# Kernel optimization log

Measured on AMD Instinct MI355X. Metric: run time of the kernel, lower is better.

## Reference

```python
import jax, jax.numpy as jnp
import numpy as np
import math

D_MODEL = 1024
NUM_HEADS = 16
D_K = D_MODEL // NUM_HEADS
NUM_BUCKETS = 32
MAX_DISTANCE = 512  # PositionalEncoding max_len


def _relative_position_bucket(relative_position):
    # Faithful to the torch code: both signs add num_buckets//2 (==16), rp==0 adds 0.
    half = NUM_BUCKETS // 2            # 16
    max_exact = NUM_BUCKETS // 4       # 8
    base = (relative_position > 0).astype(jnp.int32) * half \
         + (relative_position < 0).astype(jnp.int32) * half
    arp = jnp.abs(relative_position)
    is_small = arp < max_exact
    safe = jnp.maximum(arp, 1).astype(jnp.float32)  # avoid log(0); masked by is_small anyway
    large = max_exact + (jnp.log(safe / max_exact)
                         / math.log(MAX_DISTANCE / max_exact)
                         * (half - max_exact)).astype(jnp.int32)  # trunc == torch .long()
    large = jnp.minimum(large, half - 1)
    return base + jnp.where(is_small, arp, large)


def compute_bias(rel_bias_table, seq_length):
    ctx = jnp.arange(seq_length, dtype=jnp.int32)[:, None]
    mem = jnp.arange(seq_length, dtype=jnp.int32)[None, :]
    buckets = _relative_position_bucket(mem - ctx)        # [S, S]
    values = rel_bias_table[buckets]                       # [S, S, H]
    return jnp.transpose(values, (2, 0, 1))[None]          # [1, H, S, S]


def setup_inputs() -> dict:
    key = jax.random.key(0)
    ks = jax.random.split(key, 12)
    B, S, D = 2, 2048, D_MODEL
    scale = 1.0 / math.sqrt(D)
    inp = {
        "query": jax.random.normal(ks[0], (B, S, D), jnp.float32),
        "key": jax.random.normal(ks[1], (B, S, D), jnp.float32),
        "value": jax.random.normal(ks[2], (B, S, D), jnp.float32),
        "Wq": jax.random.normal(ks[3], (D, D), jnp.float32) * scale,
        "bq": jnp.zeros((D,), jnp.float32),
        "Wk": jax.random.normal(ks[4], (D, D), jnp.float32) * scale,
        "bk": jnp.zeros((D,), jnp.float32),
        "Wv": jax.random.normal(ks[5], (D, D), jnp.float32) * scale,
        "bv": jnp.zeros((D,), jnp.float32),
        "Wo": jax.random.normal(ks[6], (D, D), jnp.float32) * scale,
        "bo": jnp.zeros((D,), jnp.float32),
        "rel_bias_table": jax.random.normal(ks[7], (NUM_BUCKETS, NUM_HEADS), jnp.float32) * 0.1,
    }
    return inp


def reference(query, key, value, Wq, bq, Wk, bk, Wv, bv, Wo, bo, rel_bias_table):
    B, Sq, D = query.shape
    Sk = key.shape[1]
    H, dk = NUM_HEADS, D_K
    q = (query @ Wq + bq).reshape(B, Sq, H, dk)
    k = (key @ Wk + bk).reshape(B, Sk, H, dk)
    v = (value @ Wv + bv).reshape(B, Sk, H, dk)
    scores = jnp.einsum('bqhd,bkhd->bhqk', q, k) / math.sqrt(dk)  # [B,H,Sq,Sk]
    position_bias = compute_bias(rel_bias_table, max(Sq, Sk))[:, :, :Sq, :Sk]
    scores = scores + position_bias  # broadcast over batch (torch expand)
    attn_weights = jax.nn.softmax(scores, axis=-1)
    # dropout is identity in eval / p=0
    context = jnp.einsum('bhqk,bkhd->bqhd', attn_weights, v).reshape(B, Sq, D)
    output = context @ Wo + bo
    pb = jnp.broadcast_to(position_bias, (B, H, Sq, Sk))
    return output, attn_weights, pb
```

## Files before the change

### kernel.cpp

```cpp
#include <hip/hip_runtime.h>
#include <hip/hip_bf16.h>

#define BN 2
#define SEQ 2048
#define DM 1024
#define NH 16
#define DK 64

using f32x4  = __attribute__((ext_vector_type(4))) float;
using bf16x8 = __attribute__((ext_vector_type(8))) __bf16;
using short8 = __attribute__((ext_vector_type(8))) short;

static_assert(sizeof(bf16x8) == 16, "bf16x8 must be 16B");

#define MFMA16(a, b, c) __builtin_amdgcn_mfma_f32_16x16x32_bf16(a, b, c, 0, 0, 0)

__device__ __forceinline__ unsigned short f2b(float f) {
    __hip_bfloat16 h = __float2bfloat16(f);
    return __builtin_bit_cast(unsigned short, h);
}

__device__ __forceinline__ bf16x8 load_bf8(const unsigned short* p) {
    short8 s = *reinterpret_cast<const short8*>(p);
    return __builtin_bit_cast(bf16x8, s);
}

__global__ void bias_table_kernel(const float* __restrict__ rel,
                                  float* __restrict__ bias_val) {
    int idx = blockIdx.x * 256 + threadIdx.x;
    if (idx >= NH * 4095) return;
    int h = idx / 4095;
    int dd = idx - h * 4095;
    int d = dd - 2047;
    int a = d < 0 ? -d : d;
    int bucket;
    if (a == 0) bucket = 0;
    else if (a < 8) bucket = 16 + a;
    else {
        int k = (a >= 14) + (a >= 23) + (a >= 39) + (a >= 64) +
                (a >= 108) + (a >= 182) + (a >= 305);
        bucket = 24 + k;
    }
    bias_val[h * 4095 + dd] = rel[bucket * NH + h];
}

__global__ __launch_bounds__(256) void wtrans_kernel(
        const float* __restrict__ W0, const float* __restrict__ W1,
        const float* __restrict__ W2, const float* __restrict__ W3,
        unsigned short* __restrict__ T0, unsigned short* __restrict__ T1,
        unsigned short* __restrict__ T2, unsigned short* __restrict__ T3) {
    constexpr int P = 68;
    __shared__ unsigned short lt[64 * P];
    const int mz = blockIdx.z;
    const float* W = mz == 0 ? W0 : mz == 1 ? W1 : mz == 2 ? W2 : W3;
    unsigned short* T = mz == 0 ? T0 : mz == 1 ? T1 : mz == 2 ? T2 : T3;
    const int k0 = blockIdx.x * 64, n0 = blockIdx.y * 64;
    const int tid = threadIdx.x;
#pragma unroll
    for (int p = 0; p < 4; ++p) {
        int r = p * 16 + (tid >> 4);
        int c = (tid & 15) * 4;
        float4 vv = *(const float4*)&W[(size_t)(k0 + r) * DM + n0 + c];
#pragma unroll
        for (int j = 0; j < 4; ++j) {
            int n = c + j;
            float x = j == 0 ? vv.x : j == 1 ? vv.y : j == 2 ? vv.z : vv.w;
            lt[n * P + (r ^ ((n & 7) << 3))] = f2b(x);
        }
    }
    __syncthreads();
#pragma unroll
    for (int p = 0; p < 2; ++p) {
        int rn = p * 32 + (tid >> 3);
        int ck = (tid & 7) * 8;
        int ckx = ck ^ ((rn & 7) << 3);
        ushort4 a0 = *(ushort4*)&lt[rn * P + ckx];
        ushort4 a1 = *(ushort4*)&lt[rn * P + ckx + 4];
        *(ushort4*)&T[(size_t)(n0 + rn) * DM + k0 + ck] = a0;
        *(ushort4*)&T[(size_t)(n0 + rn) * DM + k0 + ck + 4] = a1;
    }
}

__global__ __launch_bounds__(256) void qkv_gemm(
        const float* __restrict__ Aq, const float* __restrict__ Ak, const float* __restrict__ Av,
        const unsigned short* __restrict__ Wtq, const unsigned short* __restrict__ Wtk,
        const unsigned short* __restrict__ Wtv,
        const float* __restrict__ bq, const float* __restrict__ bk, const float* __restrict__ bv,
        unsigned short* __restrict__ Qp, unsigned short* __restrict__ Kh,
        unsigned short* __restrict__ Vt) {
    constexpr int KP = 40;
    __shared__ unsigned short la[128 * KP];
    __shared__ unsigned short lb[128 * KP];
    const int mat = blockIdx.z;
    const float* A = mat == 0 ? Aq : mat == 1 ? Ak : Av;
    const unsigned short* Wt = mat == 0 ? Wtq : mat == 1 ? Wtk : Wtv;
    const float* bias = mat == 0 ? bq : mat == 1 ? bk : bv;
    const float outscale = mat == 0 ? 0.125f : 1.0f;
    const int tid = threadIdx.x;
    const int m0 = blockIdx.y * 128, n0 = blockIdx.x * 128;
    const int lane = tid & 63, wid = tid >> 6;
    const int wm0 = (wid >> 1) * 64, wn0 = (wid & 1) * 64;
    const int l15 = lane & 15, l4 = lane >> 4;
    f32x4 acc[4][4] = {};

    for (int kt = 0; kt < 32; ++kt) {
        const int k0 = kt * 32;
#pragma unroll
        for (int i = 0; i < 4; ++i) {
            int idx = tid + i * 256;
            int row = idx >> 3, c4 = (idx & 7) * 4;
            float4 v = *(const float4*)(A + (size_t)(m0 + row) * DM + k0 + c4);
            ushort4 u; u.x = f2b(v.x); u.y = f2b(v.y); u.z = f2b(v.z); u.w = f2b(v.w);
            *(ushort4*)&la[row * KP + c4] = u;
        }
#pragma unroll
        for (int i = 0; i < 2; ++i) {
            int idx = tid + i * 256;
            int row = idx >> 2, c8 = (idx & 3) * 8;
            *(int4*)&lb[row * KP + c8] =
                *(const int4*)&Wt[(size_t)(n0 + row) * DM + k0 + c8];
        }
        __syncthreads();
        bf16x8 af[4], bfv[4];
#pragma unroll
        for (int m = 0; m < 4; ++m)
            af[m] = load_bf8(&la[(wm0 + m * 16 + l15) * KP + l4 * 8]);
#pragma unroll
        for (int n = 0; n < 4; ++n)
            bfv[n] = load_bf8(&lb[(wn0 + n * 16 + l15) * KP + l4 * 8]);
#pragma unroll
        for (int m = 0; m < 4; ++m)
#pragma unroll
            for (int n = 0; n < 4; ++n)
                acc[m][n] = MFMA16(af[m], bfv[n], acc[m][n]);
        __syncthreads();
    }

    float bv4[4];
#pragma unroll
    for (int n = 0; n < 4; ++n) bv4[n] = bias[n0 + wn0 + n * 16 + l15];
#pragma unroll
    for (int m = 0; m < 4; ++m) {
#pragma unroll
        for (int n = 0; n < 4; ++n) {
            int gcol = n0 + wn0 + n * 16 + l15;
#pragma unroll
            for (int r = 0; r < 4; ++r) {
                int grow = m0 + wm0 + m * 16 + l4 * 4 + r;
                float val = (acc[m][n][r] + bv4[n]) * outscale;
                unsigned short ob = f2b(val);
                int b = grow >> 11, s = grow & 2047;
                int hh = gcol >> 6, dl = gcol & 63;
                if (mat == 0) {
                    Qp[(size_t)grow * DM + gcol] = ob;
                } else if (mat == 1) {
                    Kh[(((size_t)(b * NH + hh) * SEQ + s) << 6) + dl] = ob;
                } else {
                    Vt[(((size_t)(b * NH + hh) * DK + dl) << 11) + s] = ob;
                }
            }
        }
    }
}

__global__ __launch_bounds__(256) void o_gemm(
        const unsigned short* __restrict__ Actx, const unsigned short* __restrict__ Wto,
        const float* __restrict__ bo, float* __restrict__ out) {
    constexpr int KP = 40;
    __shared__ unsigned short la[64 * KP];
    __shared__ unsigned short lb[128 * KP];
    const int tid = threadIdx.x;
    const int m0 = blockIdx.y * 64, n0 = blockIdx.x * 128;
    const int lane = tid & 63, wid = tid >> 6;
    const int wm0 = (wid >> 1) * 32, wn0 = (wid & 1) * 64;
    const int l15 = lane & 15, l4 = lane >> 4;
    f32x4 acc[2][4] = {};

    for (int kt = 0; kt < 32; ++kt) {
        const int k0 = kt * 32;
        {
            int row = tid >> 2, c8 = (tid & 3) * 8;
            *(int4*)&la[row * KP + c8] =
                *(const int4*)&Actx[(size_t)(m0 + row) * DM + k0 + c8];
        }
#pragma unroll
        for (int i = 0; i < 2; ++i) {
            int idx = tid + i * 256;
            int row = idx >> 2, c8 = (idx & 3) * 8;
            *(int4*)&lb[row * KP + c8] =
                *(const int4*)&Wto[(size_t)(n0 + row) * DM + k0 + c8];
        }
        __syncthreads();
        bf16x8 af[2], bfv[4];
#pragma unroll
        for (int m = 0; m < 2; ++m)
            af[m] = load_bf8(&la[(wm0 + m * 16 + l15) * KP + l4 * 8]);
#pragma unroll
        for (int n = 0; n < 4; ++n)
            bfv[n] = load_bf8(&lb[(wn0 + n * 16 + l15) * KP + l4 * 8]);
#pragma unroll
        for (int m = 0; m < 2; ++m)
#pragma unroll
            for (int n = 0; n < 4; ++n)
                acc[m][n] = MFMA16(af[m], bfv[n], acc[m][n]);
        __syncthreads();
    }

#pragma unroll
    for (int m = 0; m < 2; ++m)
#pragma unroll
        for (int n = 0; n < 4; ++n) {
            int gcol = n0 + wn0 + n * 16 + l15;
            float bb = bo[gcol];
#pragma unroll
            for (int r = 0; r < 4; ++r) {
                int grow = m0 + wm0 + m * 16 + l4 * 4 + r;
                out[(size_t)grow * DM + gcol] = acc[m][n][r] + bb;
            }
        }
}

__global__ __launch_bounds__(256) void attn3_kernel(
        const unsigned short* __restrict__ Qp, const unsigned short* __restrict__ Kh,
        const unsigned short* __restrict__ Vt, const float* __restrict__ bias_val,
        float* __restrict__ attn_out, float* __restrict__ pb_out,
        unsigned short* __restrict__ ctx) {
    __shared__ float bias_lds[2112];
    __shared__ float wtile[4][16 * 36];
    const int tid = threadIdx.x;
    const int lane = tid & 63, wid = tid >> 6;
    const int l15 = lane & 15, l4 = lane >> 4;
    const int bid = (blockIdx.x & 7) * 128 + (blockIdx.x >> 3);
    const int qb = bid & 31;
    const int h = (bid >> 5) & 15;
    const int b = bid >> 9;
    const int q0 = qb * 64;
    const int qw = q0 + wid * 16;

    {
        const float* bp = bias_val + h * 4095 + (2047 - (q0 + 63));
        for (int i = tid; i < 2111; i += 256) bias_lds[i] = bp[i];
    }
    __syncthreads();

    const unsigned short* qbase = Qp + (size_t)(b * SEQ + qw + l15) * DM + h * DK;
    bf16x8 qa0 = load_bf8(qbase + l4 * 8);
    bf16x8 qa1 = load_bf8(qbase + 32 + l4 * 8);

    const unsigned short* kbase = Kh + (((size_t)(b * NH + h) * SEQ) << 6);
    const int bbase = 63 - wid * 16 - l4 * 4;

    float m[4], l[4];
#pragma unroll
    for (int r = 0; r < 4; ++r) { m[r] = -3e38f; l[r] = 0.f; }

    for (int c0 = 0; c0 < SEQ; c0 += 32) {
        const unsigned short* kp = kbase + ((size_t)(c0 + l15) << 6);
        bf16x8 k00 = load_bf8(kp + l4 * 8);
        bf16x8 k01 = load_bf8(kp + 32 + l4 * 8);
        bf16x8 k10 = load_bf8(kp + (16 << 6) + l4 * 8);
        bf16x8 k11 = load_bf8(kp + (16 << 6) + 32 + l4 * 8);
        f32x4 a0 = {}, a1 = {};
        a0 = MFMA16(qa0, k00, a0); a0 = MFMA16(qa1, k01, a0);
        a1 = MFMA16(qa0, k10, a1); a1 = MFMA16(qa1, k11, a1);
#pragma unroll
        for (int r = 0; r < 4; ++r) {
            float s0 = a0[r] + bias_lds[c0 + l15 + bbase - r];
            float s1 = a1[r] + bias_lds[c0 + 16 + l15 + bbase - r];
            float cm = fmaxf(s0, s1);
            if (cm > m[r]) { l[r] *= __expf(m[r] - cm); m[r] = cm; }
            l[r] += __expf(s0 - m[r]) + __expf(s1 - m[r]);
        }
    }
#pragma unroll
    for (int off = 1; off < 16; off <<= 1) {
#pragma unroll
        for (int r = 0; r < 4; ++r) {
            float om = __shfl_xor(m[r], off);
            float ol = __shfl_xor(l[r], off);
            float M = fmaxf(m[r], om);
            l[r] = l[r] * __expf(m[r] - M) + ol * __expf(om - M);
            m[r] = M;
        }
    }
    float invl[4];
#pragma unroll
    for (int r = 0; r < 4; ++r) invl[r] = 1.0f / l[r];

    float* wt = wtile[wid];
    float* abase = attn_out + ((size_t)((b * NH + h) * SEQ + qw)) * SEQ;
    float* pbase = pb_out + ((size_t)((b * NH + h) * SEQ + qw)) * SEQ;
    const unsigned short* vbase = Vt + (((size_t)(b * NH + h) * DK) << 11);
    f32x4 cacc[4] = {};

    bf16x8 k00, k01, k10, k11;
    {
        const unsigned short* kp = kbase + ((size_t)l15 << 6);
        k00 = load_bf8(kp + l4 * 8);
        k01 = load_bf8(kp + 32 + l4 * 8);
        k10 = load_bf8(kp + (16 << 6) + l4 * 8);
        k11 = load_bf8(kp + (16 << 6) + 32 + l4 * 8);
    }
    const int srow = lane >> 2, scg = (lane & 3) * 8;
    for (int c0 = 0; c0 < SEQ; c0 += 32) {
        f32x4 a0 = {}, a1 = {};
        a0 = MFMA16(qa0, k00, a0); a0 = MFMA16(qa1, k01, a0);
        a1 = MFMA16(qa0, k10, a1); a1 = MFMA16(qa1, k11, a1);
        const int cn = (c0 + 32) & (SEQ - 1);
        const unsigned short* kp = kbase + ((size_t)(cn + l15) << 6);
        k00 = load_bf8(kp + l4 * 8);
        k01 = load_bf8(kp + 32 + l4 * 8);
        k10 = load_bf8(kp + (16 << 6) + l4 * 8);
        k11 = load_bf8(kp + (16 << 6) + 32 + l4 * 8);
        bf16x8 vv0 = load_bf8(vbase + ((size_t)(0 * 16 + l15) << 11) + c0 + l4 * 8);
        bf16x8 vv1 = load_bf8(vbase + ((size_t)(1 * 16 + l15) << 11) + c0 + l4 * 8);
        bf16x8 vv2 = load_bf8(vbase + ((size_t)(2 * 16 + l15) << 11) + c0 + l4 * 8);
        bf16x8 vv3 = load_bf8(vbase + ((size_t)(3 * 16 + l15) << 11) + c0 + l4 * 8);
#pragma unroll
        for (int r = 0; r < 4; ++r) {
            int row = l4 * 4 + r;
            float w0 = __expf(a0[r] + bias_lds[c0 + l15 + bbase - r] - m[r]) * invl[r];
            float w1 = __expf(a1[r] + bias_lds[c0 + 16 + l15 + bbase - r] - m[r]) * invl[r];
            wt[row * 36 + l15] = w0;
            wt[row * 36 + 16 + l15] = w1;
        }
        asm volatile("s_waitcnt lgkmcnt(0)" ::: "memory");
        __builtin_amdgcn_sched_barrier(0);
        {
            float4 v0 = *(const float4*)&wt[srow * 36 + scg];
            float4 v1 = *(const float4*)&wt[srow * 36 + scg + 4];
            float* gp = abase + (size_t)srow * SEQ + c0 + scg;
            *(float4*)gp = v0;
            *(float4*)(gp + 4) = v1;
        }
        {
            const int ib = c0 + scg + bbase + l4 * 4 - srow;
            float4 p0, p1;
            p0.x = bias_lds[ib + 0]; p0.y = bias_lds[ib + 1];
            p0.z = bias_lds[ib + 2]; p0.w = bias_lds[ib + 3];
            p1.x = bias_lds[ib + 4]; p1.y = bias_lds[ib + 5];
            p1.z = bias_lds[ib + 6]; p1.w = bias_lds[ib + 7];
            float* gp = pbase + (size_t)srow * SEQ + c0 + scg;
            *(float4*)gp = p0;
            *(float4*)(gp + 4) = p1;
        }
        float4 pA = *(const float4*)&wt[l15 * 36 + l4 * 8];
        float4 pB = *(const float4*)&wt[l15 * 36 + l4 * 8 + 4];
        short8 ps;
        ps[0] = (short)f2b(pA.x); ps[1] = (short)f2b(pA.y);
        ps[2] = (short)f2b(pA.z); ps[3] = (short)f2b(pA.w);
        ps[4] = (short)f2b(pB.x); ps[5] = (short)f2b(pB.y);
        ps[6] = (short)f2b(pB.z); ps[7] = (short)f2b(pB.w);
        bf16x8 pf = __builtin_bit_cast(bf16x8, ps);
        cacc[0] = MFMA16(pf, vv0, cacc[0]);
        cacc[1] = MFMA16(pf, vv1, cacc[1]);
        cacc[2] = MFMA16(pf, vv2, cacc[2]);
        cacc[3] = MFMA16(pf, vv3, cacc[3]);
        asm volatile("s_waitcnt lgkmcnt(0)" ::: "memory");
        __builtin_amdgcn_sched_barrier(0);
    }
#pragma unroll
    for (int d0 = 0; d0 < 4; ++d0)
#pragma unroll
        for (int r = 0; r < 4; ++r)
            ctx[(size_t)(b * SEQ + qw + l4 * 4 + r) * DM + h * DK + d0 * 16 + l15] =
                f2b(cacc[d0][r]);
}

extern "C" void kernel_launch(void* const* d_in, const int* in_sizes, int n_in,
                              void* d_out, int out_size, void* d_ws, size_t ws_size,
                              hipStream_t stream) {
    const float* query = (const float*)d_in[0];
    const float* key   = (const float*)d_in[1];
    const float* value = (const float*)d_in[2];
    const float* Wq = (const float*)d_in[3];
    const float* bq = (const float*)d_in[4];
    const float* Wk = (const float*)d_in[5];
    const float* bk = (const float*)d_in[6];
    const float* Wv = (const float*)d_in[7];
    const float* bv = (const float*)d_in[8];
    const float* Wo = (const float*)d_in[9];
    const float* bo = (const float*)d_in[10];
    const float* rel = (const float*)d_in[11];

    float* out = (float*)d_out;
    float* attn_out = out + (size_t)BN * SEQ * DM;
    float* pb_out = attn_out + (size_t)BN * NH * SEQ * SEQ;

    char* ws = (char*)d_ws;
    float* bias_val = (float*)ws;
    unsigned short* Qp  = (unsigned short*)(ws + 262144);
    unsigned short* Kh  = Qp + (size_t)BN * SEQ * DM;
    unsigned short* Vt  = Kh + (size_t)BN * SEQ * DM;
    unsigned short* ctx = Vt + (size_t)BN * SEQ * DM;
    unsigned short* Wtq = ctx + (size_t)BN * SEQ * DM;
    unsigned short* Wtk = Wtq + (size_t)DM * DM;
    unsigned short* Wtv = Wtk + (size_t)DM * DM;
    unsigned short* Wto = Wtv + (size_t)DM * DM;

    bias_table_kernel<<<256, 256, 0, stream>>>(rel, bias_val);
    wtrans_kernel<<<dim3(16, 16, 4), 256, 0, stream>>>(Wq, Wk, Wv, Wo, Wtq, Wtk, Wtv, Wto);
    qkv_gemm<<<dim3(8, 32, 3), 256, 0, stream>>>(query, key, value, Wtq, Wtk, Wtv,
                                                 bq, bk, bv, Qp, Kh, Vt);
    attn3_kernel<<<BN * NH * (SEQ / 64), 256, 0, stream>>>(Qp, Kh, Vt, bias_val,
                                                           attn_out, pb_out, ctx);
    o_gemm<<<dim3(8, 64), 256, 0, stream>>>(ctx, Wto, bo, out);
}
```

Baseline: 601.0 us.

## Replace online softmax max pass with Cauchy-Schwarz upper bound and fused PV pass

The QKV GEMM epilogue now computes per-row query norms and a per-head maximum key norm via atomicMax, and the attention kernel uses their product plus the bias maximum as a fixed softmax shift instead of a running max. This lets the first pass accumulate both the row sum and the P·V product in one sweep, with the probabilities exchanged through lane shuffles instead of an LDS tile. The second pass recomputes the scores only to write normalized attention weights and the bias directly from registers. It drops the separate statistics pass and the LDS round trip, but relies on the bound being tight enough to avoid underflow in exp. It also writes attention rows with a different store pattern.

```diff
diff --git a/kernel.cpp b/kernel.cpp
--- a/kernel.cpp
+++ b/kernel.cpp
@@ -26,8 +26,10 @@
 }
 
 __global__ void bias_table_kernel(const float* __restrict__ rel,
-                                  float* __restrict__ bias_val) {
+                                  float* __restrict__ bias_val,
+                                  unsigned int* __restrict__ khmax) {
     int idx = blockIdx.x * 256 + threadIdx.x;
+    if (blockIdx.x == 0 && threadIdx.x < BN * NH) khmax[threadIdx.x] = 0u;
     if (idx >= NH * 4095) return;
     int h = idx / 4095;
     int dd = idx - h * 4095;
@@ -87,7 +89,8 @@
         const unsigned short* __restrict__ Wtv,
         const float* __restrict__ bq, const float* __restrict__ bk, const float* __restrict__ bv,
         unsigned short* __restrict__ Qp, unsigned short* __restrict__ Kh,
-        unsigned short* __restrict__ Vt) {
+        unsigned short* __restrict__ Vt,
+        float* __restrict__ qnorm, unsigned int* __restrict__ khmax) {
     constexpr int KP = 40;
     __shared__ unsigned short la[128 * KP];
     __shared__ unsigned short lb[128 * KP];
@@ -139,6 +142,12 @@
     float bv4[4];
 #pragma unroll
     for (int n = 0; n < 4; ++n) bv4[n] = bias[n0 + wn0 + n * 16 + l15];
+    float nsq[4][4];
+#pragma unroll
+    for (int m = 0; m < 4; ++m)
+#pragma unroll
+        for (int r = 0; r < 4; ++r) nsq[m][r] = 0.f;
+
 #pragma unroll
     for (int m = 0; m < 4; ++m) {
 #pragma unroll
@@ -148,6 +157,7 @@
             for (int r = 0; r < 4; ++r) {
                 int grow = m0 + wm0 + m * 16 + l4 * 4 + r;
                 float val = (acc[m][n][r] + bv4[n]) * outscale;
+                nsq[m][r] += val * val;
                 unsigned short ob = f2b(val);
                 int b = grow >> 11, s = grow & 2047;
                 int hh = gcol >> 6, dl = gcol & 63;
@@ -160,6 +170,28 @@
                 }
             }
         }
+    }
+    if (mat < 2) {
+        const int hh = (n0 + wn0) >> 6;
+#pragma unroll
+        for (int m = 0; m < 4; ++m)
+#pragma unroll
+            for (int r = 0; r < 4; ++r) {
+                float s2 = nsq[m][r];
+                s2 += __shfl_xor(s2, 1);
+                s2 += __shfl_xor(s2, 2);
+                s2 += __shfl_xor(s2, 4);
+                s2 += __shfl_xor(s2, 8);
+                if (l15 == 0) {
+                    int grow = m0 + wm0 + m * 16 + l4 * 4 + r;
+                    int b = grow >> 11, s = grow & 2047;
+                    float nrm = sqrtf(s2);
+                    if (mat == 0)
+                        qnorm[(b * NH + hh) * SEQ + s] = nrm;
+                    else
+                        atomicMax(&khmax[b * NH + hh], __float_as_uint(nrm));
+                }
+            }
     }
 }
 
@@ -220,13 +252,14 @@
         }
 }
 
-__global__ __launch_bounds__(256) void attn3_kernel(
+__global__ __launch_bounds__(256) void attn4_kernel(
         const unsigned short* __restrict__ Qp, const unsigned short* __restrict__ Kh,
         const unsigned short* __restrict__ Vt, const float* __restrict__ bias_val,
+        const float* __restrict__ qnorm, const unsigned int* __restrict__ khmax,
         float* __restrict__ attn_out, float* __restrict__ pb_out,
         unsigned short* __restrict__ ctx) {
     __shared__ float bias_lds[2112];
-    __shared__ float wtile[4][16 * 36];
+    __shared__ float redmax[4];
     const int tid = threadIdx.x;
     const int lane = tid & 63, wid = tid >> 6;
     const int l15 = lane & 15, l4 = lane >> 4;
@@ -236,135 +269,122 @@
     const int b = bid >> 9;
     const int q0 = qb * 64;
     const int qw = q0 + wid * 16;
-
+    const int bh = b * NH + h;
+
+    float pmax = -1e30f;
     {
         const float* bp = bias_val + h * 4095 + (2047 - (q0 + 63));
-        for (int i = tid; i < 2111; i += 256) bias_lds[i] = bp[i];
-    }
+        for (int i = tid; i < 2111; i += 256) {
+            float x = bp[i];
+            bias_lds[i] = x;
+            pmax = fmaxf(pmax, x);
+        }
+    }
+#pragma unroll
+    for (int off = 1; off < 64; off <<= 1) pmax = fmaxf(pmax, __shfl_xor(pmax, off));
+    if (lane == 0) redmax[wid] = pmax;
     __syncthreads();
+    const float bmax = fmaxf(fmaxf(redmax[0], redmax[1]), fmaxf(redmax[2], redmax[3]));
+
+    const float M = qnorm[bh * SEQ + qw + l15] * 1.01f * __uint_as_float(khmax[bh])
+                    + bmax + 0.1f;
 
     const unsigned short* qbase = Qp + (size_t)(b * SEQ + qw + l15) * DM + h * DK;
     bf16x8 qa0 = load_bf8(qbase + l4 * 8);
     bf16x8 qa1 = load_bf8(qbase + 32 + l4 * 8);
-
-    const unsigned short* kbase = Kh + (((size_t)(b * NH + h) * SEQ) << 6);
-    const int bbase = 63 - wid * 16 - l4 * 4;
-
-    float m[4], l[4];
-#pragma unroll
-    for (int r = 0; r < 4; ++r) { m[r] = -3e38f; l[r] = 0.f; }
-
+    const unsigned short* kbase = Kh + (((size_t)bh * SEQ) << 6);
+    const unsigned short* vbase = Vt + (((size_t)bh * DK) << 11);
+    const int ibb = 63 - wid * 16 - l15 + l4 * 4;
+
+    float lsum = 0.f;
+    f32x4 cacc[4] = {};
+    const int sa = l15 + (((2 * l4) & 3) << 4);
+    const int sb = sa + 16;
     for (int c0 = 0; c0 < SEQ; c0 += 32) {
         const unsigned short* kp = kbase + ((size_t)(c0 + l15) << 6);
-        bf16x8 k00 = load_bf8(kp + l4 * 8);
-        bf16x8 k01 = load_bf8(kp + 32 + l4 * 8);
-        bf16x8 k10 = load_bf8(kp + (16 << 6) + l4 * 8);
-        bf16x8 k11 = load_bf8(kp + (16 << 6) + 32 + l4 * 8);
-        f32x4 a0 = {}, a1 = {};
-        a0 = MFMA16(qa0, k00, a0); a0 = MFMA16(qa1, k01, a0);
-        a1 = MFMA16(qa0, k10, a1); a1 = MFMA16(qa1, k11, a1);
-#pragma unroll
-        for (int r = 0; r < 4; ++r) {
-            float s0 = a0[r] + bias_lds[c0 + l15 + bbase - r];
-            float s1 = a1[r] + bias_lds[c0 + 16 + l15 + bbase - r];
-            float cm = fmaxf(s0, s1);
-            if (cm > m[r]) { l[r] *= __expf(m[r] - cm); m[r] = cm; }
-            l[r] += __expf(s0 - m[r]) + __expf(s1 - m[r]);
-        }
-    }
-#pragma unroll
-    for (int off = 1; off < 16; off <<= 1) {
-#pragma unroll
-        for (int r = 0; r < 4; ++r) {
-            float om = __shfl_xor(m[r], off);
-            float ol = __shfl_xor(l[r], off);
-            float M = fmaxf(m[r], om);
-            l[r] = l[r] * __expf(m[r] - M) + ol * __expf(om - M);
-            m[r] = M;
-        }
-    }
-    float invl[4];
-#pragma unroll
-    for (int r = 0; r < 4; ++r) invl[r] = 1.0f / l[r];
-
-    float* wt = wtile[wid];
-    float* abase = attn_out + ((size_t)((b * NH + h) * SEQ + qw)) * SEQ;
-    float* pbase = pb_out + ((size_t)((b * NH + h) * SEQ + qw)) * SEQ;
-    const unsigned short* vbase = Vt + (((size_t)(b * NH + h) * DK) << 11);
-    f32x4 cacc[4] = {};
-
-    bf16x8 k00, k01, k10, k11;
-    {
-        const unsigned short* kp = kbase + ((size_t)l15 << 6);
-        k00 = load_bf8(kp + l4 * 8);
-        k01 = load_bf8(kp + 32 + l4 * 8);
-        k10 = load_bf8(kp + (16 << 6) + l4 * 8);
-        k11 = load_bf8(kp + (16 << 6) + 32 + l4 * 8);
-    }
-    const int srow = lane >> 2, scg = (lane & 3) * 8;
-    for (int c0 = 0; c0 < SEQ; c0 += 32) {
-        f32x4 a0 = {}, a1 = {};
-        a0 = MFMA16(qa0, k00, a0); a0 = MFMA16(qa1, k01, a0);
-        a1 = MFMA16(qa0, k10, a1); a1 = MFMA16(qa1, k11, a1);
-        const int cn = (c0 + 32) & (SEQ - 1);
-        const unsigned short* kp = kbase + ((size_t)(cn + l15) << 6);
-        k00 = load_bf8(kp + l4 * 8);
-        k01 = load_bf8(kp + 32 + l4 * 8);
-        k10 = load_bf8(kp + (16 << 6) + l4 * 8);
-        k11 = load_bf8(kp + (16 << 6) + 32 + l4 * 8);
+        bf16x8 kb0 = load_bf8(kp + l4 * 8);
+        bf16x8 kb1 = load_bf8(kp + 32 + l4 * 8);
+        bf16x8 kb2 = load_bf8(kp + (16 << 6) + l4 * 8);
+        bf16x8 kb3 = load_bf8(kp + (16 << 6) + 32 + l4 * 8);
         bf16x8 vv0 = load_bf8(vbase + ((size_t)(0 * 16 + l15) << 11) + c0 + l4 * 8);
         bf16x8 vv1 = load_bf8(vbase + ((size_t)(1 * 16 + l15) << 11) + c0 + l4 * 8);
         bf16x8 vv2 = load_bf8(vbase + ((size_t)(2 * 16 + l15) << 11) + c0 + l4 * 8);
         bf16x8 vv3 = load_bf8(vbase + ((size_t)(3 * 16 + l15) << 11) + c0 + l4 * 8);
+        f32x4 a0 = {}, a1 = {};
+        a0 = MFMA16(kb0, qa0, a0); a0 = MFMA16(kb1, qa1, a0);
+        a1 = MFMA16(kb2, qa0, a1); a1 = MFMA16(kb3, qa1, a1);
+        float e[8];
 #pragma unroll
         for (int r = 0; r < 4; ++r) {
-            int row = l4 * 4 + r;
-            float w0 = __expf(a0[r] + bias_lds[c0 + l15 + bbase - r] - m[r]) * invl[r];
-            float w1 = __expf(a1[r] + bias_lds[c0 + 16 + l15 + bbase - r] - m[r]) * invl[r];
-            wt[row * 36 + l15] = w0;
-            wt[row * 36 + 16 + l15] = w1;
-        }
-        asm volatile("s_waitcnt lgkmcnt(0)" ::: "memory");
-        __builtin_amdgcn_sched_barrier(0);
-        {
-            float4 v0 = *(const float4*)&wt[srow * 36 + scg];
-            float4 v1 = *(const float4*)&wt[srow * 36 + scg + 4];
-            float* gp = abase + (size_t)srow * SEQ + c0 + scg;
-            *(float4*)gp = v0;
-            *(float4*)(gp + 4) = v1;
-        }
-        {
-            const int ib = c0 + scg + bbase + l4 * 4 - srow;
-            float4 p0, p1;
-            p0.x = bias_lds[ib + 0]; p0.y = bias_lds[ib + 1];
-            p0.z = bias_lds[ib + 2]; p0.w = bias_lds[ib + 3];
-            p1.x = bias_lds[ib + 4]; p1.y = bias_lds[ib + 5];
-            p1.z = bias_lds[ib + 6]; p1.w = bias_lds[ib + 7];
-            float* gp = pbase + (size_t)srow * SEQ + c0 + scg;
-            *(float4*)gp = p0;
-            *(float4*)(gp + 4) = p1;
-        }
-        float4 pA = *(const float4*)&wt[l15 * 36 + l4 * 8];
-        float4 pB = *(const float4*)&wt[l15 * 36 + l4 * 8 + 4];
-        short8 ps;
-        ps[0] = (short)f2b(pA.x); ps[1] = (short)f2b(pA.y);
-        ps[2] = (short)f2b(pA.z); ps[3] = (short)f2b(pA.w);
-        ps[4] = (short)f2b(pB.x); ps[5] = (short)f2b(pB.y);
-        ps[6] = (short)f2b(pB.z); ps[7] = (short)f2b(pB.w);
-        bf16x8 pf = __builtin_bit_cast(bf16x8, ps);
+            e[r]     = __expf(a0[r] + bias_lds[c0 + r + ibb] - M);
+            e[4 + r] = __expf(a1[r] + bias_lds[c0 + 16 + r + ibb] - M);
+        }
+        lsum += ((e[0] + e[1]) + (e[2] + e[3])) + ((e[4] + e[5]) + (e[6] + e[7]));
+        unsigned u0 = ((unsigned)f2b(e[1]) << 16) | f2b(e[0]);
+        unsigned u1 = ((unsigned)f2b(e[3]) << 16) | f2b(e[2]);
+        unsigned u2 = ((unsigned)f2b(e[5]) << 16) | f2b(e[4]);
+        unsigned u3 = ((unsigned)f2b(e[7]) << 16) | f2b(e[6]);
+        unsigned A0 = (unsigned)__shfl((int)u0, sa), A1 = (unsigned)__shfl((int)u1, sa);
+        unsigned A2 = (unsigned)__shfl((int)u2, sa), A3 = (unsigned)__shfl((int)u3, sa);
+        unsigned B0 = (unsigned)__shfl((int)u0, sb), B1 = (unsigned)__shfl((int)u1, sb);
+        unsigned B2 = (unsigned)__shfl((int)u2, sb), B3 = (unsigned)__shfl((int)u3, sb);
+        const bool lo = l4 < 2;
+        uint4 wv;
+        wv.x = lo ? A0 : A2;
+        wv.y = lo ? A1 : A3;
+        wv.z = lo ? B0 : B2;
+        wv.w = lo ? B1 : B3;
+        bf16x8 pf = __builtin_bit_cast(bf16x8, wv);
         cacc[0] = MFMA16(pf, vv0, cacc[0]);
         cacc[1] = MFMA16(pf, vv1, cacc[1]);
         cacc[2] = MFMA16(pf, vv2, cacc[2]);
         cacc[3] = MFMA16(pf, vv3, cacc[3]);
-        asm volatile("s_waitcnt lgkmcnt(0)" ::: "memory");
-        __builtin_amdgcn_sched_barrier(0);
-    }
+    }
+    lsum += __shfl_xor(lsum, 16);
+    lsum += __shfl_xor(lsum, 32);
+    const float invl = 1.0f / lsum;
+    const float Mlog = M + __logf(lsum);
+
+    float invr[4];
+#pragma unroll
+    for (int r = 0; r < 4; ++r) invr[r] = __shfl(invl, l4 * 4 + r);
 #pragma unroll
     for (int d0 = 0; d0 < 4; ++d0)
 #pragma unroll
         for (int r = 0; r < 4; ++r)
             ctx[(size_t)(b * SEQ + qw + l4 * 4 + r) * DM + h * DK + d0 * 16 + l15] =
-                f2b(cacc[d0][r]);
+                f2b(cacc[d0][r] * invr[r]);
+
+    float* abase = attn_out + ((size_t)(bh * SEQ + qw + l15)) * SEQ;
+    float* pbase = pb_out + ((size_t)(bh * SEQ + qw + l15)) * SEQ;
+    for (int c0 = 0; c0 < SEQ; c0 += 32) {
+        const unsigned short* kp = kbase + ((size_t)(c0 + l15) << 6);
+        bf16x8 kb0 = load_bf8(kp + l4 * 8);
+        bf16x8 kb1 = load_bf8(kp + 32 + l4 * 8);
+        bf16x8 kb2 = load_bf8(kp + (16 << 6) + l4 * 8);
+        bf16x8 kb3 = load_bf8(kp + (16 << 6) + 32 + l4 * 8);
+        f32x4 a0 = {}, a1 = {};
+        a0 = MFMA16(kb0, qa0, a0); a0 = MFMA16(kb1, qa1, a0);
+        a1 = MFMA16(kb2, qa0, a1); a1 = MFMA16(kb3, qa1, a1);
+        float4 b0, b1;
+        b0.x = bias_lds[c0 + 0 + ibb]; b0.y = bias_lds[c0 + 1 + ibb];
+        b0.z = bias_lds[c0 + 2 + ibb]; b0.w = bias_lds[c0 + 3 + ibb];
+        b1.x = bias_lds[c0 + 16 + ibb]; b1.y = bias_lds[c0 + 17 + ibb];
+        b1.z = bias_lds[c0 + 18 + ibb]; b1.w = bias_lds[c0 + 19 + ibb];
+        float4 f0, f1;
+        f0.x = __expf(a0[0] + b0.x - Mlog);
+        f0.y = __expf(a0[1] + b0.y - Mlog);
+        f0.z = __expf(a0[2] + b0.z - Mlog);
+        f0.w = __expf(a0[3] + b0.w - Mlog);
+        f1.x = __expf(a1[0] + b1.x - Mlog);
+        f1.y = __expf(a1[1] + b1.y - Mlog);
+        f1.z = __expf(a1[2] + b1.z - Mlog);
+        f1.w = __expf(a1[3] + b1.w - Mlog);
+        *(float4*)(abase + c0 + l4 * 4) = f0;
+        *(float4*)(abase + c0 + 16 + l4 * 4) = f1;
+        *(float4*)(pbase + c0 + l4 * 4) = b0;
+        *(float4*)(pbase + c0 + 16 + l4 * 4) = b1;
+    }
 }
 
 extern "C" void kernel_launch(void* const* d_in, const int* in_sizes, int n_in,
@@ -397,12 +417,15 @@
     unsigned short* Wtk = Wtq + (size_t)DM * DM;
     unsigned short* Wtv = Wtk + (size_t)DM * DM;
     unsigned short* Wto = Wtv + (size_t)DM * DM;
-
-    bias_table_kernel<<<256, 256, 0, stream>>>(rel, bias_val);
+    float* qnorm = (float*)(Wto + (size_t)DM * DM);
+    unsigned int* khmax = (unsigned int*)(qnorm + (size_t)BN * NH * SEQ);
+
+    bias_table_kernel<<<256, 256, 0, stream>>>(rel, bias_val, khmax);
     wtrans_kernel<<<dim3(16, 16, 4), 256, 0, stream>>>(Wq, Wk, Wv, Wo, Wtq, Wtk, Wtv, Wto);
     qkv_gemm<<<dim3(8, 32, 3), 256, 0, stream>>>(query, key, value, Wtq, Wtk, Wtv,
-                                                 bq, bk, bv, Qp, Kh, Vt);
-    attn3_kernel<<<BN * NH * (SEQ / 64), 256, 0, stream>>>(Qp, Kh, Vt, bias_val,
+                                                 bq, bk, bv, Qp, Kh, Vt, qnorm, khmax);
+    attn4_kernel<<<BN * NH * (SEQ / 64), 256, 0, stream>>>(Qp, Kh, Vt, bias_val,
+                                                           qnorm, khmax,
                                                            attn_out, pb_out, ctx);
     o_gemm<<<dim3(8, 64), 256, 0, stream>>>(ctx, Wto, bo, out);
 }
```

New measurement: 1.056 ms. +75.8%, slower.
